# Kernel tuning notes

Hardware: AMD Instinct MI355X
Metric: run time of the kernel (lower is better)

The kernel has to match this reference:

```python
import jax, jax.numpy as jnp
import numpy as np

N_NODES = 100000
N_EDGES = 3200000
STATE_DIM = 128
HIDDEN = 256
ACTION_DIM = 64
BN_EPS = 1e-5


def setup_inputs() -> dict:
    key = jax.random.key(0)
    ks = jax.random.split(key, 12)
    feat = jax.random.normal(ks[0], (N_NODES, STATE_DIM), dtype=jnp.float32)
    src = jax.random.randint(ks[1], (N_EDGES,), 0, N_NODES, dtype=jnp.int64) if jax.config.jax_enable_x64 else jax.random.randint(ks[1], (N_EDGES,), 0, N_NODES).astype(jnp.int32)
    dst = jax.random.randint(ks[2], (N_EDGES,), 0, N_NODES).astype(src.dtype)
    def glorot(k, shape):
        lim = np.sqrt(6.0 / (shape[0] + shape[1]))
        return jax.random.uniform(k, shape, jnp.float32, -lim, lim)
    W1 = glorot(ks[3], (STATE_DIM, HIDDEN)); b1 = jnp.zeros((HIDDEN,), jnp.float32)
    W2 = glorot(ks[4], (HIDDEN, HIDDEN));   b2 = jnp.zeros((HIDDEN,), jnp.float32)
    g1 = jnp.ones((HIDDEN,), jnp.float32);  be1 = jnp.zeros((HIDDEN,), jnp.float32)
    g2 = jnp.ones((HIDDEN,), jnp.float32);  be2 = jnp.zeros((HIDDEN,), jnp.float32)
    Wa = glorot(ks[5], (HIDDEN, ACTION_DIM)); ba = jnp.zeros((ACTION_DIM,), jnp.float32)
    Wv = glorot(ks[6], (HIDDEN, 1));          bv = jnp.zeros((1,), jnp.float32)
    return {"feat": feat, "src": src, "dst": dst, "W1": W1, "b1": b1, "g1": g1, "be1": be1,
            "W2": W2, "b2": b2, "g2": g2, "be2": be2, "Wa": Wa, "ba": ba, "Wv": Wv, "bv": bv}


def _graph_conv(x, src, dst, dnorm_out, dnorm_in, W, b):
    # DGL GraphConv, norm='both': scale by out-deg^{-1/2} at src, sum-aggregate at dst,
    # scale by in-deg^{-1/2}, then linear.
    m = x * dnorm_out[:, None]                     # [N, F]
    agg = jax.ops.segment_sum(m[src], dst, num_segments=N_NODES)  # SpMM
    h = agg * dnorm_in[:, None]
    return h @ W + b


def _bn_relu(x, gamma, beta):
    mu = x.mean(axis=0)
    var = x.var(axis=0)  # biased, matches torch BN training normalization
    return jax.nn.relu((x - mu) * jax.lax.rsqrt(var + BN_EPS) * gamma + beta)


def reference(feat, src, dst, W1, b1, g1, be1, W2, b2, g2, be2, Wa, ba, Wv, bv):
    ones = jnp.ones((src.shape[0],), feat.dtype)
    deg_out = jax.ops.segment_sum(ones, src, num_segments=N_NODES)
    deg_in = jax.ops.segment_sum(ones, dst, num_segments=N_NODES)
    dnorm_out = jax.lax.rsqrt(jnp.clip(deg_out, 1.0))
    dnorm_in = jax.lax.rsqrt(jnp.clip(deg_in, 1.0))
    h = _bn_relu(_graph_conv(feat, src, dst, dnorm_out, dnorm_in, W1, b1), g1, be1)
    h = _bn_relu(_graph_conv(h, src, dst, dnorm_out, dnorm_in, W2, b2), g2, be2)
    adv = h @ Wa + ba                              # [N, A]
    val = h @ Wv + bv                              # [N, 1]
    Q = val + (adv - adv.mean(axis=1, keepdims=True))
    return Q
```

## Files before the change

### kernel.cpp

```cpp
#include <hip/hip_runtime.h>
#include <hip/hip_bf16.h>

#define NN 100000
#define NE 3200000
#define HID 256
#define SDIM 128
#define ADIM 64
#define BN_EPS 1e-5f

#define BSH 9
#define NB 196
#define EPB 16384
#define NAB 196
#define CAP 24576

typedef __attribute__((ext_vector_type(8))) short short8;
typedef __attribute__((ext_vector_type(4))) float f32x4;

__device__ __forceinline__ void atomAdd(float* p, float v) { unsafeAtomicAdd(p, v); }
__device__ __forceinline__ float bf2f(ushort u) {
    union { unsigned i; float f; } c; c.i = ((unsigned)u) << 16; return c.f;
}
__device__ __forceinline__ ushort f2bf(float x) {
    __hip_bfloat16 h = __float2bfloat16(x);
    return *reinterpret_cast<ushort*>(&h);
}

__global__ __launch_bounds__(1024)
void k_hist(const int* __restrict__ src, const int* __restrict__ dst,
            unsigned* __restrict__ gh_d, unsigned* __restrict__ gh_s, int E) {
    __shared__ unsigned hd[NB], hs[NB];
    int tid = threadIdx.x;
    if (tid < NB) { hd[tid] = 0; hs[tid] = 0; }
    __syncthreads();
    int base = blockIdx.x * EPB;
    int cnt = min(EPB, E - base);
    for (int i = tid; i < cnt; i += 1024) {
        atomicAdd(&hd[dst[base + i] >> BSH], 1u);
        atomicAdd(&hs[src[base + i] >> BSH], 1u);
    }
    __syncthreads();
    if (tid < NB) {
        if (hd[tid]) atomicAdd(&gh_d[tid * 16], hd[tid]);
        if (hs[tid]) atomicAdd(&gh_s[tid * 16], hs[tid]);
    }
}

__global__ __launch_bounds__(256)
void k_scan_b(const unsigned* __restrict__ gh_d, const unsigned* __restrict__ gh_s,
              unsigned* __restrict__ gcur_d, unsigned* __restrict__ gcur_s,
              unsigned* __restrict__ bbase_d, unsigned* __restrict__ bbase_s,
              int* __restrict__ row_ptr) {
    __shared__ unsigned v[256];
    int t = threadIdx.x;
    unsigned x = (t < NB) ? gh_d[t * 16] : 0;
    v[t] = x; __syncthreads();
    for (int off = 1; off < 256; off <<= 1) {
        unsigned a = (t >= off) ? v[t - off] : 0;
        __syncthreads(); v[t] += a; __syncthreads();
    }
    if (t < NB) { bbase_d[t] = v[t] - x; gcur_d[t * 16] = v[t] - x; }
    if (t == 255) { bbase_d[NB] = v[255]; row_ptr[NN] = (int)v[255]; }
    __syncthreads();
    unsigned y = (t < NB) ? gh_s[t * 16] : 0;
    v[t] = y; __syncthreads();
    for (int off = 1; off < 256; off <<= 1) {
        unsigned a = (t >= off) ? v[t - off] : 0;
        __syncthreads(); v[t] += a; __syncthreads();
    }
    if (t < NB) { bbase_s[t] = v[t] - y; gcur_s[t * 16] = v[t] - y; }
    if (t == 255) bbase_s[NB] = v[255];
}

__global__ __launch_bounds__(1024)
void k_part(const int* __restrict__ src, const int* __restrict__ dst,
            unsigned* __restrict__ gcur_d, unsigned* __restrict__ gcur_s,
            unsigned* __restrict__ outd, ushort* __restrict__ outs, int E) {
    __shared__ unsigned hd[NB], hs[NB], ld_[NB], ls_[NB], cd[NB], cs[NB], bd[NB], bs[NB];
    __shared__ unsigned sv[256];
    __shared__ unsigned stage_d[EPB];
    __shared__ ushort stage_s[EPB];
    __shared__ unsigned char sbd[EPB], sbs[EPB];
    const int tid = threadIdx.x;
    const int base = blockIdx.x * EPB;
    const int cnt = min(EPB, E - base);
    if (tid < NB) { hd[tid] = 0; hs[tid] = 0; }
    __syncthreads();

    int es[16], ed[16];
    #pragma unroll
    for (int i = 0; i < 16; ++i) {
        int g = tid + i * 1024;
        if (g < cnt) { es[i] = src[base + g]; ed[i] = dst[base + g]; }
        else { es[i] = -1; ed[i] = -1; }
    }
    #pragma unroll
    for (int i = 0; i < 16; ++i)
        if (ed[i] >= 0) {
            atomicAdd(&hd[ed[i] >> BSH], 1u);
            atomicAdd(&hs[es[i] >> BSH], 1u);
        }
    __syncthreads();

    {
        unsigned x = (tid < NB) ? hd[tid] : 0;
        if (tid < 256) sv[tid] = x;
        __syncthreads();
        for (int off = 1; off < 256; off <<= 1) {
            unsigned a = 0;
            if (tid < 256 && tid >= off) a = sv[tid - off];
            __syncthreads();
            if (tid < 256) sv[tid] += a;
            __syncthreads();
        }
        if (tid < NB) {
            ld_[tid] = sv[tid] - x; cd[tid] = sv[tid] - x;
            bd[tid] = atomicAdd(&gcur_d[tid * 16], hd[tid]);
        }
        __syncthreads();
        unsigned y = (tid < NB) ? hs[tid] : 0;
        if (tid < 256) sv[tid] = y;
        __syncthreads();
        for (int off = 1; off < 256; off <<= 1) {
            unsigned a = 0;
            if (tid < 256 && tid >= off) a = sv[tid - off];
            __syncthreads();
            if (tid < 256) sv[tid] += a;
            __syncthreads();
        }
        if (tid < NB) {
            ls_[tid] = sv[tid] - y; cs[tid] = sv[tid] - y;
            bs[tid] = atomicAdd(&gcur_s[tid * 16], hs[tid]);
        }
        __syncthreads();
    }

    #pragma unroll
    for (int i = 0; i < 16; ++i)
        if (ed[i] >= 0) {
            int b = ed[i] >> BSH;
            unsigned p = atomicAdd(&cd[b], 1u);
            stage_d[p] = ((unsigned)(ed[i] & ((1 << BSH) - 1)) << 17) | (unsigned)es[i];
            sbd[p] = (unsigned char)b;
            int b2 = es[i] >> BSH;
            unsigned p2 = atomicAdd(&cs[b2], 1u);
            stage_s[p2] = (ushort)(es[i] & ((1 << BSH) - 1));
            sbs[p2] = (unsigned char)b2;
        }
    __syncthreads();

    for (int i = tid; i < cnt; i += 1024) {
        unsigned b = sbd[i];
        outd[bd[b] + (unsigned)i - ld_[b]] = stage_d[i];
        unsigned b2 = sbs[i];
        outs[bs[b2] + (unsigned)i - ls_[b2]] = stage_s[i];
    }
}

__global__ __launch_bounds__(1024)
void k_csr(const unsigned* __restrict__ outd, const unsigned* __restrict__ bbase_d,
           int* __restrict__ row_ptr, int* __restrict__ csr_src, float* __restrict__ dni) {
    __shared__ unsigned h[512], sc[512];
    __shared__ int sorted[CAP];
    const int tid = threadIdx.x, b = blockIdx.x;
    const unsigned beg = bbase_d[b], end = bbase_d[b + 1];
    const int cnt = (int)(end - beg);
    if (tid < 512) h[tid] = 0;
    __syncthreads();
    for (int i = tid; i < cnt; i += 1024) atomicAdd(&h[outd[beg + i] >> 17], 1u);
    __syncthreads();
    unsigned my = 0;
    if (tid < 512) { my = h[tid]; sc[tid] = my; }
    __syncthreads();
    for (int off = 1; off < 512; off <<= 1) {
        unsigned a = 0;
        if (tid < 512 && tid >= off) a = sc[tid - off];
        __syncthreads();
        if (tid < 512) sc[tid] += a;
        __syncthreads();
    }
    const int n0 = b << BSH;
    const int nb = min(512, NN - n0);
    unsigned excl = 0;
    if (tid < 512) excl = sc[tid] - my;
    __syncthreads();
    if (tid < 512) h[tid] = excl;
    if (tid < nb) {
        row_ptr[n0 + tid] = (int)(beg + excl);
        dni[n0 + tid] = rsqrtf(fmaxf((float)my, 1.0f));
    }
    __syncthreads();
    for (int i = tid; i < cnt; i += 1024) {
        unsigned p = outd[beg + i];
        unsigned pos = atomicAdd(&h[p >> 17], 1u);
        sorted[pos] = (int)(p & 0x1FFFFu);
    }
    __syncthreads();
    for (int i = tid; i < cnt; i += 1024) csr_src[beg + i] = sorted[i];
}

__global__ __launch_bounds__(1024)
void k_degout(const ushort* __restrict__ outs, const unsigned* __restrict__ bbase_s,
              float* __restrict__ dno) {
    __shared__ unsigned h[512];
    const int tid = threadIdx.x, b = blockIdx.x;
    const unsigned beg = bbase_s[b], end = bbase_s[b + 1];
    const int cnt = (int)(end - beg);
    if (tid < 512) h[tid] = 0;
    __syncthreads();
    for (int i = tid; i < cnt; i += 1024) atomicAdd(&h[outs[beg + i]], 1u);
    __syncthreads();
    const int n0 = b << BSH;
    const int nb = min(512, NN - n0);
    if (tid < nb) dno[n0 + tid] = rsqrtf(fmaxf((float)h[tid], 1.0f));
}

__global__ __launch_bounds__(256)
void k_wt(const float* __restrict__ W, ushort* __restrict__ Wt, int K, int N) {
    int idx = blockIdx.x * 256 + threadIdx.x;
    if (idx >= K * N) return;
    int n = idx / K, k = idx - n * K;
    Wt[idx] = f2bf(W[(size_t)k * N + n]);
}

__global__ __launch_bounds__(256)
void k_wth(const float* __restrict__ Wa, const float* __restrict__ Wv,
           ushort* __restrict__ Wh) {
    int idx = blockIdx.x * 256 + threadIdx.x;
    if (idx >= 80 * HID) return;
    int n = idx / HID, k = idx - n * HID;
    float v = 0.f;
    if (n < ADIM) v = Wa[(size_t)k * ADIM + n];
    else if (n == ADIM) v = Wv[k];
    Wh[idx] = f2bf(v);
}

__global__ __launch_bounds__(256)
void k_prescale_cvt(const float* __restrict__ X, const float* __restrict__ dno,
                    ushort* __restrict__ Y, int total4) {
    int idx = blockIdx.x * 256 + threadIdx.x;
    if (idx >= total4) return;
    int row = idx >> 5;
    float s = dno[row];
    float4 v = reinterpret_cast<const float4*>(X)[idx];
    ushort4 o;
    o.x = f2bf(v.x * s); o.y = f2bf(v.y * s);
    o.z = f2bf(v.z * s); o.w = f2bf(v.w * s);
    reinterpret_cast<ushort4*>(Y)[idx] = o;
}

template <int F>
__global__ __launch_bounds__(256)
void k_spmm_bf16(const int* __restrict__ row_ptr, const int* __restrict__ csr_src,
                 const ushort* __restrict__ X, const float* __restrict__ dni,
                 ushort* __restrict__ Y, int N) {
    const int node = blockIdx.x * 4 + (threadIdx.x >> 6);
    if (node >= N) return;
    const int lane = threadIdx.x & 63;
    const int beg = row_ptr[node];
    const int end = row_ptr[node + 1];
    float acc[4] = {0.f, 0.f, 0.f, 0.f};

    if (F == 256) {
        const ushort* Xl = X + lane * 4;
        int e = beg;
        for (; e + 1 < end; e += 2) {
            int s0 = csr_src[e];
            int s1 = csr_src[e + 1];
            ushort4 v0 = *reinterpret_cast<const ushort4*>(Xl + (size_t)s0 * 256);
            ushort4 v1 = *reinterpret_cast<const ushort4*>(Xl + (size_t)s1 * 256);
            acc[0] += bf2f(v0.x) + bf2f(v1.x);
            acc[1] += bf2f(v0.y) + bf2f(v1.y);
            acc[2] += bf2f(v0.z) + bf2f(v1.z);
            acc[3] += bf2f(v0.w) + bf2f(v1.w);
        }
        if (e < end) {
            int s0 = csr_src[e];
            ushort4 v0 = *reinterpret_cast<const ushort4*>(Xl + (size_t)s0 * 256);
            acc[0] += bf2f(v0.x); acc[1] += bf2f(v0.y);
            acc[2] += bf2f(v0.z); acc[3] += bf2f(v0.w);
        }
        float wi = dni[node];
        ushort4 o;
        o.x = f2bf(acc[0] * wi); o.y = f2bf(acc[1] * wi);
        o.z = f2bf(acc[2] * wi); o.w = f2bf(acc[3] * wi);
        *reinterpret_cast<ushort4*>(Y + (size_t)node * 256 + lane * 4) = o;
    } else {
        const int half = lane >> 5;
        const int l = lane & 31;
        const ushort* Xl = X + l * 4;
        for (int e = beg + half; e < end; e += 2) {
            int s = csr_src[e];
            ushort4 v = *reinterpret_cast<const ushort4*>(Xl + (size_t)s * 128);
            acc[0] += bf2f(v.x); acc[1] += bf2f(v.y);
            acc[2] += bf2f(v.z); acc[3] += bf2f(v.w);
        }
        acc[0] += __shfl_xor(acc[0], 32);
        acc[1] += __shfl_xor(acc[1], 32);
        acc[2] += __shfl_xor(acc[2], 32);
        acc[3] += __shfl_xor(acc[3], 32);
        if (half == 0) {
            float wi = dni[node];
            ushort4 o;
            o.x = f2bf(acc[0] * wi); o.y = f2bf(acc[1] * wi);
            o.z = f2bf(acc[2] * wi); o.w = f2bf(acc[3] * wi);
            *reinterpret_cast<ushort4*>(Y + (size_t)node * 128 + l * 4) = o;
        }
    }
}

template <int K>
__global__ __launch_bounds__(256, 2)
void k_gemm_mfma(const ushort* __restrict__ A, const ushort* __restrict__ Wt,
                 const float* __restrict__ bias, ushort* __restrict__ outb,
                 float* __restrict__ stats, int M) {
    __shared__ ushort As[128][40];
    __shared__ ushort Bs[256][40];
    __shared__ float sred[4][2][128];
    const int tid = threadIdx.x;
    const int w = tid >> 6;
    const int lane = tid & 63;
    const int wr = (w >> 1) * 64;
    const int wc = (w & 1) * 128;
    const int row0 = blockIdx.x * 128;
    f32x4 acc[4][8] = {};

    const int frow = lane & 15;
    const int fk = (lane >> 4) * 8;

    for (int k0 = 0; k0 < K; k0 += 32) {
        #pragma unroll
        for (int h = 0; h < 2; ++h) {
            int slot = tid + 256 * h;
            int r = slot >> 2;
            int c = (slot & 3) * 8;
            int row = row0 + r;
            int4 v = make_int4(0, 0, 0, 0);
            if (row < M) v = *reinterpret_cast<const int4*>(A + (size_t)row * K + k0 + c);
            *reinterpret_cast<int4*>(&As[r][c]) = v;
        }
        #pragma unroll
        for (int h = 0; h < 4; ++h) {
            int slot = tid + 256 * h;
            int n = slot >> 2;
            int c = (slot & 3) * 8;
            int4 v = *reinterpret_cast<const int4*>(Wt + (size_t)n * K + k0 + c);
            *reinterpret_cast<int4*>(&Bs[n][c]) = v;
        }
        __syncthreads();

        short8 afr[4], bfr[8];
        #pragma unroll
        for (int mi = 0; mi < 4; ++mi)
            afr[mi] = *reinterpret_cast<const short8*>(&As[wr + mi * 16 + frow][fk]);
        #pragma unroll
        for (int ni = 0; ni < 8; ++ni)
            bfr[ni] = *reinterpret_cast<const short8*>(&Bs[wc + ni * 16 + frow][fk]);
        #pragma unroll
        for (int mi = 0; mi < 4; ++mi)
            #pragma unroll
            for (int ni = 0; ni < 8; ++ni)
                acc[mi][ni] = __builtin_amdgcn_mfma_f32_16x16x32_bf16(afr[mi], bfr[ni], acc[mi][ni], 0, 0, 0);
        __syncthreads();
    }

    const int ncol = lane & 15;
    const int rbase = (lane >> 4) * 4;
    #pragma unroll
    for (int ni = 0; ni < 8; ++ni) {
        int col = wc + ni * 16 + ncol;
        float b = bias[col];
        float s1 = 0.f, s2 = 0.f;
        #pragma unroll
        for (int mi = 0; mi < 4; ++mi) {
            #pragma unroll
            for (int q = 0; q < 4; ++q) {
                int row = row0 + wr + mi * 16 + rbase + q;
                if (row < M) {
                    float val = acc[mi][ni][q] + b;
                    outb[(size_t)row * HID + col] = f2bf(val);
                    s1 += val;
                    s2 += val * val;
                }
            }
        }
        s1 += __shfl_xor(s1, 16); s1 += __shfl_xor(s1, 32);
        s2 += __shfl_xor(s2, 16); s2 += __shfl_xor(s2, 32);
        if ((lane >> 4) == 0) {
            sred[w][0][ni * 16 + ncol] = s1;
            sred[w][1][ni * 16 + ncol] = s2;
        }
    }
    __syncthreads();
    {
        int c = tid;
        int half = c >> 7, cl = c & 127;
        float v0 = sred[half][0][cl] + sred[half + 2][0][cl];
        float v1 = sred[half][1][cl] + sred[half + 2][1][cl];
        atomAdd(&stats[c], v0);
        atomAdd(&stats[HID + c], v1);
    }
}

__global__ __launch_bounds__(256)
void k_bn_relu_ps(const ushort* __restrict__ Gb, const float* __restrict__ stats,
                  const float* __restrict__ gamma, const float* __restrict__ beta,
                  const float* __restrict__ dno, ushort* __restrict__ Y, int total8) {
    int idx = blockIdx.x * 256 + threadIdx.x;
    if (idx >= total8) return;
    int row = idx >> 5;
    int c0 = (idx & 31) * 8;
    short8 v = *reinterpret_cast<const short8*>(Gb + (size_t)idx * 8);
    float s = dno[row];
    float inv_n = 1.0f / (float)NN;
    short8 o;
    #pragma unroll
    for (int j = 0; j < 8; ++j) {
        int c = c0 + j;
        float mean = stats[c] * inv_n;
        float var = stats[HID + c] * inv_n - mean * mean;
        float sc = gamma[c] * rsqrtf(var + BN_EPS);
        float sh = beta[c] - mean * sc;
        float x = bf2f((ushort)v[j]);
        float y = fmaf(x, sc, sh);
        y = y > 0.f ? y : 0.f;
        o[j] = (short)f2bf(y * s);
    }
    *reinterpret_cast<short8*>(Y + (size_t)idx * 8) = o;
}

__global__ __launch_bounds__(256)
void k_bn_qhead(const ushort* __restrict__ Gb, const float* __restrict__ stats,
                const float* __restrict__ gamma, const float* __restrict__ beta,
                const ushort* __restrict__ Wh, const float* __restrict__ ba,
                const float* __restrict__ bv, float* __restrict__ out, int M) {
    __shared__ ushort As[128][40];
    __shared__ ushort Bs[80][264];
    __shared__ float sc_s[HID], sh_s[HID];
    const int tid = threadIdx.x;
    const int w = tid >> 6;
    const int lane = tid & 63;
    const int row0 = blockIdx.x * 128;
    const int frow = lane & 15;
    const int fk8 = (lane >> 4) * 8;

    {
        float inv_n = 1.0f / (float)NN;
        float mean = stats[tid] * inv_n;
        float var = stats[HID + tid] * inv_n - mean * mean;
        float sc = gamma[tid] * rsqrtf(var + BN_EPS);
        sc_s[tid] = sc;
        sh_s[tid] = beta[tid] - mean * sc;
    }
    #pragma unroll
    for (int h = 0; h < 10; ++h) {
        int slot = tid + 256 * h;
        int n = slot >> 5;
        int c = (slot & 31) * 8;
        int4 v = *reinterpret_cast<const int4*>(Wh + (size_t)n * HID + c);
        *reinterpret_cast<int4*>(&Bs[n][c]) = v;
    }
    __syncthreads();

    f32x4 acc[2][5] = {};
    for (int k0 = 0; k0 < HID; k0 += 32) {
        #pragma unroll
        for (int h = 0; h < 2; ++h) {
            int slot = tid + 256 * h;
            int r = slot >> 2;
            int c = (slot & 3) * 8;
            int row = row0 + r;
            short8 o = {};
            if (row < M) {
                short8 v = *reinterpret_cast<const short8*>(Gb + (size_t)row * HID + k0 + c);
                #pragma unroll
                for (int j = 0; j < 8; ++j) {
                    int k = k0 + c + j;
                    float y = fmaf(bf2f((ushort)v[j]), sc_s[k], sh_s[k]);
                    o[j] = (short)f2bf(y > 0.f ? y : 0.f);
                }
            }
            *reinterpret_cast<short8*>(&As[r][c]) = o;
        }
        __syncthreads();
        short8 afr[2], bfr[5];
        #pragma unroll
        for (int mi = 0; mi < 2; ++mi)
            afr[mi] = *reinterpret_cast<const short8*>(&As[w * 32 + mi * 16 + frow][fk8]);
        #pragma unroll
        for (int ni = 0; ni < 5; ++ni)
            bfr[ni] = *reinterpret_cast<const short8*>(&Bs[ni * 16 + frow][k0 + fk8]);
        #pragma unroll
        for (int mi = 0; mi < 2; ++mi)
            #pragma unroll
            for (int ni = 0; ni < 5; ++ni)
                acc[mi][ni] = __builtin_amdgcn_mfma_f32_16x16x32_bf16(afr[mi], bfr[ni], acc[mi][ni], 0, 0, 0);
        __syncthreads();
    }

    const int ncol = lane & 15;
    const int gb = lane & 48;
    const float bv0 = bv[0];
    float ba_l[4];
    #pragma unroll
    for (int ni = 0; ni < 4; ++ni) ba_l[ni] = ba[ni * 16 + ncol];
    #pragma unroll
    for (int mi = 0; mi < 2; ++mi) {
        #pragma unroll
        for (int q = 0; q < 4; ++q) {
            int row = row0 + w * 32 + mi * 16 + (lane >> 4) * 4 + q;
            float adv[4];
            float s = 0.f;
            #pragma unroll
            for (int ni = 0; ni < 4; ++ni) {
                adv[ni] = acc[mi][ni][q] + ba_l[ni];
                s += adv[ni];
            }
            s += __shfl_xor(s, 1); s += __shfl_xor(s, 2);
            s += __shfl_xor(s, 4); s += __shfl_xor(s, 8);
            float mean = s * (1.0f / ADIM);
            float val = acc[mi][4][q] + bv0;
            val = __shfl(val, gb);
            if (row < M) {
                #pragma unroll
                for (int ni = 0; ni < 4; ++ni)
                    out[(size_t)row * ADIM + ni * 16 + ncol] = val + adv[ni] - mean;
            }
        }
    }
}

extern "C" void kernel_launch(void* const* d_in, const int* in_sizes, int n_in,
                              void* d_out, int out_size, void* d_ws, size_t ws_size,
                              hipStream_t stream) {
    const float* feat = (const float*)d_in[0];
    const int* src = (const int*)d_in[1];
    const int* dst = (const int*)d_in[2];
    const float* W1 = (const float*)d_in[3];
    const float* b1 = (const float*)d_in[4];
    const float* g1 = (const float*)d_in[5];
    const float* be1 = (const float*)d_in[6];
    const float* W2 = (const float*)d_in[7];
    const float* b2 = (const float*)d_in[8];
    const float* g2 = (const float*)d_in[9];
    const float* be2 = (const float*)d_in[10];
    const float* Wa = (const float*)d_in[11];
    const float* ba = (const float*)d_in[12];
    const float* Wv = (const float*)d_in[13];
    const float* bv = (const float*)d_in[14];
    float* out = (float*)d_out;

    char* w = (char*)d_ws;
    unsigned* gh_d   = (unsigned*)w;  w += (size_t)NB * 16 * 4;
    unsigned* gh_s   = (unsigned*)w;  w += (size_t)NB * 16 * 4;
    float* stats     = (float*)w;     w += 1024 * 4;
    unsigned* gcur_d = (unsigned*)w;  w += (size_t)NB * 16 * 4;
    unsigned* gcur_s = (unsigned*)w;  w += (size_t)NB * 16 * 4;
    unsigned* bbase_d= (unsigned*)w;  w += (NB + 4) * 4;
    unsigned* bbase_s= (unsigned*)w;  w += (NB + 4) * 4;
    float* dn_out    = (float*)w;     w += (size_t)NN * 4;
    float* dn_in     = (float*)w;     w += (size_t)NN * 4;
    int* row_ptr     = (int*)w;       w += (size_t)(NN + 4) * 4;
    unsigned* outd   = (unsigned*)w;  w += (size_t)NE * 4;
    ushort* outs     = (ushort*)w;    w += (size_t)NE * 2;
    int* csr_src     = (int*)w;       w += (size_t)NE * 4;
    ushort* Wt1      = (ushort*)w;    w += (size_t)HID * SDIM * 2;
    ushort* Wt2      = (ushort*)w;    w += (size_t)HID * HID * 2;
    ushort* Whb      = (ushort*)w;    w += (size_t)80 * HID * 2;
    ushort* Xb       = (ushort*)w;    w += (size_t)NN * HID * 2;
    ushort* Ab       = (ushort*)w;    w += (size_t)NN * HID * 2;
    ushort* Gb       = (ushort*)w;    w += (size_t)NN * HID * 2;

    hipMemsetAsync(gh_d, 0, (size_t)2 * NB * 16 * 4 + 1024 * 4, stream);

    k_hist<<<NAB, 1024, 0, stream>>>(src, dst, gh_d, gh_s, NE);
    k_scan_b<<<1, 256, 0, stream>>>(gh_d, gh_s, gcur_d, gcur_s, bbase_d, bbase_s, row_ptr);
    k_part<<<NAB, 1024, 0, stream>>>(src, dst, gcur_d, gcur_s, outd, outs, NE);
    k_csr<<<NB, 1024, 0, stream>>>(outd, bbase_d, row_ptr, csr_src, dn_in);
    k_degout<<<NB, 1024, 0, stream>>>(outs, bbase_s, dn_out);

    k_wt<<<(SDIM * HID + 255) / 256, 256, 0, stream>>>(W1, Wt1, SDIM, HID);
    k_wt<<<(HID * HID + 255) / 256, 256, 0, stream>>>(W2, Wt2, HID, HID);
    k_wth<<<(80 * HID + 255) / 256, 256, 0, stream>>>(Wa, Wv, Whb);

    const int gblocks = (NN + 127) / 128;

    {
        int t4 = NN * (SDIM / 4);
        k_prescale_cvt<<<(t4 + 255) / 256, 256, 0, stream>>>(feat, dn_out, Xb, t4);
        k_spmm_bf16<SDIM><<<(NN + 3) / 4, 256, 0, stream>>>(row_ptr, csr_src, Xb, dn_in, Ab, NN);
        k_gemm_mfma<SDIM><<<gblocks, 256, 0, stream>>>(Ab, Wt1, b1, Gb, stats, NN);
        int t8 = NN * (HID / 8);
        k_bn_relu_ps<<<(t8 + 255) / 256, 256, 0, stream>>>(Gb, stats, g1, be1, dn_out, Xb, t8);
    }

    {
        k_spmm_bf16<HID><<<(NN + 3) / 4, 256, 0, stream>>>(row_ptr, csr_src, Xb, dn_in, Ab, NN);
        k_gemm_mfma<HID><<<gblocks, 256, 0, stream>>>(Ab, Wt2, b2, Gb, stats + 512, NN);
        k_bn_qhead<<<gblocks, 256, 0, stream>>>(Gb, stats + 512, g2, be2, Whb, ba, bv, out, NN);
    }
}
```

Baseline: 740.2 us.

## Fuse preprocessing kernels, halve partition block size, scatter CSR directly

```diff
diff --git a/kernel.cpp b/kernel.cpp
--- a/kernel.cpp
+++ b/kernel.cpp
@@ -10,9 +10,8 @@
 
 #define BSH 9
 #define NB 196
-#define EPB 16384
-#define NAB 196
-#define CAP 24576
+#define EPB 8192
+#define NAB 391
 
 typedef __attribute__((ext_vector_type(8))) short short8;
 typedef __attribute__((ext_vector_type(4))) float f32x4;
@@ -87,15 +86,15 @@
     if (tid < NB) { hd[tid] = 0; hs[tid] = 0; }
     __syncthreads();
 
-    int es[16], ed[16];
-    #pragma unroll
-    for (int i = 0; i < 16; ++i) {
+    int es[8], ed[8];
+    #pragma unroll
+    for (int i = 0; i < 8; ++i) {
         int g = tid + i * 1024;
         if (g < cnt) { es[i] = src[base + g]; ed[i] = dst[base + g]; }
         else { es[i] = -1; ed[i] = -1; }
     }
     #pragma unroll
-    for (int i = 0; i < 16; ++i)
+    for (int i = 0; i < 8; ++i)
         if (ed[i] >= 0) {
             atomicAdd(&hd[ed[i] >> BSH], 1u);
             atomicAdd(&hs[es[i] >> BSH], 1u);
@@ -136,7 +135,7 @@
     }
 
     #pragma unroll
-    for (int i = 0; i < 16; ++i)
+    for (int i = 0; i < 8; ++i)
         if (ed[i] >= 0) {
             int b = ed[i] >> BSH;
             unsigned p = atomicAdd(&cd[b], 1u);
@@ -161,7 +160,6 @@
 void k_csr(const unsigned* __restrict__ outd, const unsigned* __restrict__ bbase_d,
            int* __restrict__ row_ptr, int* __restrict__ csr_src, float* __restrict__ dni) {
     __shared__ unsigned h[512], sc[512];
-    __shared__ int sorted[CAP];
     const int tid = threadIdx.x, b = blockIdx.x;
     const unsigned beg = bbase_d[b], end = bbase_d[b + 1];
     const int cnt = (int)(end - beg);
@@ -193,16 +191,16 @@
     for (int i = tid; i < cnt; i += 1024) {
         unsigned p = outd[beg + i];
         unsigned pos = atomicAdd(&h[p >> 17], 1u);
-        sorted[pos] = (int)(p & 0x1FFFFu);
-    }
-    __syncthreads();
-    for (int i = tid; i < cnt; i += 1024) csr_src[beg + i] = sorted[i];
+        csr_src[beg + pos] = (int)(p & 0x1FFFFu);
+    }
 }
 
 __global__ __launch_bounds__(1024)
-void k_degout(const ushort* __restrict__ outs, const unsigned* __restrict__ bbase_s,
-              float* __restrict__ dno) {
+void k_degout_ps(const ushort* __restrict__ outs, const unsigned* __restrict__ bbase_s,
+                 const float* __restrict__ feat, float* __restrict__ dno,
+                 ushort* __restrict__ Xb) {
     __shared__ unsigned h[512];
+    __shared__ float dnl[512];
     const int tid = threadIdx.x, b = blockIdx.x;
     const unsigned beg = bbase_s[b], end = bbase_s[b + 1];
     const int cnt = (int)(end - beg);
@@ -212,41 +210,44 @@
     __syncthreads();
     const int n0 = b << BSH;
     const int nb = min(512, NN - n0);
-    if (tid < nb) dno[n0 + tid] = rsqrtf(fmaxf((float)h[tid], 1.0f));
+    if (tid < nb) {
+        float d = rsqrtf(fmaxf((float)h[tid], 1.0f));
+        dno[n0 + tid] = d;
+        dnl[tid] = d;
+    }
+    __syncthreads();
+    const int total4 = nb * 32;
+    for (int slot = tid; slot < total4; slot += 1024) {
+        int r = slot >> 5, c4 = slot & 31;
+        float s = dnl[r];
+        float4 v = reinterpret_cast<const float4*>(feat)[(size_t)(n0 + r) * 32 + c4];
+        ushort4 o;
+        o.x = f2bf(v.x * s); o.y = f2bf(v.y * s);
+        o.z = f2bf(v.z * s); o.w = f2bf(v.w * s);
+        reinterpret_cast<ushort4*>(Xb)[(size_t)(n0 + r) * 32 + c4] = o;
+    }
 }
 
 __global__ __launch_bounds__(256)
-void k_wt(const float* __restrict__ W, ushort* __restrict__ Wt, int K, int N) {
+void k_wprep(const float* __restrict__ W1, const float* __restrict__ W2,
+             const float* __restrict__ Wa, const float* __restrict__ Wv,
+             ushort* __restrict__ Wt1, ushort* __restrict__ Wt2, ushort* __restrict__ Wh) {
     int idx = blockIdx.x * 256 + threadIdx.x;
-    if (idx >= K * N) return;
-    int n = idx / K, k = idx - n * K;
-    Wt[idx] = f2bf(W[(size_t)k * N + n]);
-}
-
-__global__ __launch_bounds__(256)
-void k_wth(const float* __restrict__ Wa, const float* __restrict__ Wv,
-           ushort* __restrict__ Wh) {
-    int idx = blockIdx.x * 256 + threadIdx.x;
-    if (idx >= 80 * HID) return;
-    int n = idx / HID, k = idx - n * HID;
-    float v = 0.f;
-    if (n < ADIM) v = Wa[(size_t)k * ADIM + n];
-    else if (n == ADIM) v = Wv[k];
-    Wh[idx] = f2bf(v);
-}
-
-__global__ __launch_bounds__(256)
-void k_prescale_cvt(const float* __restrict__ X, const float* __restrict__ dno,
-                    ushort* __restrict__ Y, int total4) {
-    int idx = blockIdx.x * 256 + threadIdx.x;
-    if (idx >= total4) return;
-    int row = idx >> 5;
-    float s = dno[row];
-    float4 v = reinterpret_cast<const float4*>(X)[idx];
-    ushort4 o;
-    o.x = f2bf(v.x * s); o.y = f2bf(v.y * s);
-    o.z = f2bf(v.z * s); o.w = f2bf(v.w * s);
-    reinterpret_cast<ushort4*>(Y)[idx] = o;
+    if (idx < HID * SDIM) {
+        int n = idx / SDIM, k = idx - n * SDIM;
+        Wt1[idx] = f2bf(W1[(size_t)k * HID + n]);
+    } else if (idx < HID * SDIM + HID * HID) {
+        int j = idx - HID * SDIM;
+        int n = j / HID, k = j - n * HID;
+        Wt2[j] = f2bf(W2[(size_t)k * HID + n]);
+    } else if (idx < HID * SDIM + HID * HID + 80 * HID) {
+        int j = idx - HID * SDIM - HID * HID;
+        int n = j / HID, k = j - n * HID;
+        float v = 0.f;
+        if (n < ADIM) v = Wa[(size_t)k * ADIM + n];
+        else if (n == ADIM) v = Wv[k];
+        Wh[j] = f2bf(v);
+    }
 }
 
 template <int F>
@@ -573,21 +574,20 @@
 
     hipMemsetAsync(gh_d, 0, (size_t)2 * NB * 16 * 4 + 1024 * 4, stream);
 
+    {
+        int total = HID * SDIM + HID * HID + 80 * HID;
+        k_wprep<<<(total + 255) / 256, 256, 0, stream>>>(W1, W2, Wa, Wv, Wt1, Wt2, Whb);
+    }
+
     k_hist<<<NAB, 1024, 0, stream>>>(src, dst, gh_d, gh_s, NE);
     k_scan_b<<<1, 256, 0, stream>>>(gh_d, gh_s, gcur_d, gcur_s, bbase_d, bbase_s, row_ptr);
     k_part<<<NAB, 1024, 0, stream>>>(src, dst, gcur_d, gcur_s, outd, outs, NE);
     k_csr<<<NB, 1024, 0, stream>>>(outd, bbase_d, row_ptr, csr_src, dn_in);
-    k_degout<<<NB, 1024, 0, stream>>>(outs, bbase_s, dn_out);
-
-    k_wt<<<(SDIM * HID + 255) / 256, 256, 0, stream>>>(W1, Wt1, SDIM, HID);
-    k_wt<<<(HID * HID + 255) / 256, 256, 0, stream>>>(W2, Wt2, HID, HID);
-    k_wth<<<(80 * HID + 255) / 256, 256, 0, stream>>>(Wa, Wv, Whb);
+    k_degout_ps<<<NB, 1024, 0, stream>>>(outs, bbase_s, feat, dn_out, Xb);
 
     const int gblocks = (NN + 127) / 128;
 
     {
-        int t4 = NN * (SDIM / 4);
-        k_prescale_cvt<<<(t4 + 255) / 256, 256, 0, stream>>>(feat, dn_out, Xb, t4);
         k_spmm_bf16<SDIM><<<(NN + 3) / 4, 256, 0, stream>>>(row_ptr, csr_src, Xb, dn_in, Ab, NN);
         k_gemm_mfma<SDIM><<<gblocks, 256, 0, stream>>>(Ab, Wt1, b1, Gb, stats, NN);
         int t8 = NN * (HID / 8);
```

After: 749.7 us. No clear change (+1.3%).
